# Kernel tuning notes

Hardware: AMD Instinct MI355X
Metric: run time of the kernel (lower is better)

The kernel has to match this reference:

```python
import jax, jax.numpy as jnp
import numpy as np

C_REG = 50.0  # soft-SVM regularization from __init__ default C=50


def kronecker(A, B):
    # torch: einsum('ab,cd->acbd').view(a*c, b*d)
    return jnp.einsum('ab,cd->acbd', A, B).reshape(
        A.shape[0] * B.shape[0], A.shape[1] * B.shape[1])


def setup_inputs() -> dict:
    key = jax.random.key(0)
    k1, k2, k3, k4 = jax.random.split(key, 4)
    N_c, N_S, N_Q, C, W, H = 16, 25, 15, 3, 32, 32
    D_feat = 640
    S_k = jax.random.normal(k1, (N_c, N_S, C, W, H), dtype=jnp.float32)
    Q_k = jax.random.normal(k2, (N_c, N_Q, C, W, H), dtype=jnp.float32)
    # base_net modeled as Flatten -> Linear(C*W*H, D_feat), no bias
    W_base = jax.random.normal(k3, (C * W * H, D_feat), dtype=jnp.float32) * 0.02
    gamma = jax.random.normal(k4, (1,), dtype=jnp.float32)
    return {"S_k": S_k, "Q_k": Q_k, "W_base": W_base, "gamma": gamma}


def reference(S_k, Q_k, W_base, gamma):
    N_c, N_S = S_k.shape[:2]
    N_Q = Q_k.shape[1]
    # base_net: flatten image dims, project to features
    f_x = S_k.reshape(N_c * N_S, -1) @ W_base  # placeholder
    f_x = Q_k.reshape(N_c * N_Q, -1) @ W_base          # [N_c*N_Q, D]
    K = S_k.reshape(N_c * N_S, -1) @ W_base            # [N_c*N_S, D]
    # kernel matrix + ridge
    aul = K @ K.T + C_REG * jnp.eye(N_c * N_S, dtype=K.dtype)  # [N_c*N_S, N_c*N_S]
    # explicit Kronecker expansion to the full (N_c^2*N_S) system
    Q = kronecker(jnp.eye(N_c, dtype=K.dtype), aul)    # [N_c^2*N_S, N_c^2*N_S]
    p = kronecker(jnp.eye(N_c, dtype=K.dtype),
                  jnp.ones((1, N_S), dtype=K.dtype)).reshape(-1, 1)
    alpha = jnp.linalg.solve(Q, jax.lax.stop_gradient(p))  # p is detached in torch
    alpha = alpha.reshape(N_c, -1)                     # [N_c, N_c*N_S]
    w_k = alpha @ K                                    # [N_c, D]
    logits = -gamma * (f_x @ w_k.T)                    # [N_c*N_Q, N_c]
    return logits
```

## Files before the change

kernel.cpp:

```cpp
#include <hip/hip_runtime.h>
#include <math.h>

#define DIN 3072
#define DF 640
#define MROWS 400
#define QROWS 240
#define NMAT 400
#define PN 416
#define NRHS 16
#define CREG 50.0f
#define PVSTEPS 5
#define CSTEPS 25
#define KSPLIT 8
#define GBLK 13
#define SCOLS 32
#define FPAD 72
#define MTILES 28
#define DPAD 424

typedef __attribute__((ext_vector_type(8))) short bf8v;
typedef __attribute__((ext_vector_type(4))) short s4v;
typedef __attribute__((ext_vector_type(4))) float f32x4;

__device__ __forceinline__ short bf16_rn(float x) {
  unsigned u = __float_as_uint(x);
  u += 0x7FFFu + ((u >> 16) & 1u);
  return (short)(u >> 16);
}
__device__ __forceinline__ void split_sh(float x, short& h, short& l) {
  h = bf16_rn(x);
  float hf = __uint_as_float(((unsigned)(unsigned short)h) << 16);
  l = bf16_rn(x - hf);
}

__global__ __launch_bounds__(256) void gemm_feat_sk(const float* __restrict__ S,
                                                    const float* __restrict__ Qm,
                                                    const float* __restrict__ Wb,
                                                    float* __restrict__ Acc) {
  __shared__ short Ash[128][FPAD];
  __shared__ short Asl[128][FPAD];
  __shared__ short Bsh[128][FPAD];
  __shared__ short Bsl[128][FPAD];
  int tid = threadIdx.x;
  int wave = tid >> 6, lane = tid & 63, l16 = lane & 15, quad = lane >> 4;
  int wr = wave >> 1, wc = wave & 1;
  int by = blockIdx.y, bx = blockIdx.x, bz = blockIdx.z;
  int colBase = bx * 128;
  int kbeg = bz * (DIN / KSPLIT), kend = kbeg + (DIN / KSPLIT);
  int kc4 = (tid & 15) * 4;
  float4 ar4[8], br4[8];
  auto load_regs = [&](int kk) {
#pragma unroll
    for (int p = 0; p < 8; ++p) {
      int ar_ = by * 128 + (tid >> 4) + 16 * p;
      const float* srp = (ar_ < MROWS) ? (S + (size_t)ar_ * DIN)
                                       : (Qm + (size_t)(ar_ - MROWS) * DIN);
      ar4[p] = *reinterpret_cast<const float4*>(srp + kk + kc4);
      int kr = (tid >> 4) + 16 * (p & 3);
      int cb = colBase + (p >> 2) * 64 + kc4;
      br4[p] = *reinterpret_cast<const float4*>(Wb + (size_t)(kk + kr) * DF + cb);
    }
  };
  auto split_write = [&]() {
#pragma unroll
    for (int p = 0; p < 8; ++p) {
      int row = (tid >> 4) + 16 * p;
      s4v hv, lv; short h, l;
      split_sh(ar4[p].x, h, l); hv[0] = h; lv[0] = l;
      split_sh(ar4[p].y, h, l); hv[1] = h; lv[1] = l;
      split_sh(ar4[p].z, h, l); hv[2] = h; lv[2] = l;
      split_sh(ar4[p].w, h, l); hv[3] = h; lv[3] = l;
      *reinterpret_cast<s4v*>(&Ash[row][kc4]) = hv;
      *reinterpret_cast<s4v*>(&Asl[row][kc4]) = lv;
      int kr = (tid >> 4) + 16 * (p & 3);
      int cb = (p >> 2) * 64 + kc4;
      split_sh(br4[p].x, h, l); Bsh[cb + 0][kr] = h; Bsl[cb + 0][kr] = l;
      split_sh(br4[p].y, h, l); Bsh[cb + 1][kr] = h; Bsl[cb + 1][kr] = l;
      split_sh(br4[p].z, h, l); Bsh[cb + 2][kr] = h; Bsl[cb + 2][kr] = l;
      split_sh(br4[p].w, h, l); Bsh[cb + 3][kr] = h; Bsl[cb + 3][kr] = l;
    }
  };
  f32x4 acc[4][4];
#pragma unroll
  for (int m = 0; m < 4; ++m)
#pragma unroll
    for (int n = 0; n < 4; ++n) acc[m][n] = {0, 0, 0, 0};
  load_regs(kbeg);
  split_write();
  __syncthreads();
  int k0 = kbeg;
  while (true) {
    int kn = k0 + 64;
    bool more = (kn < kend);
    if (more) load_regs(kn);
#pragma unroll
    for (int kk = 0; kk < 64; kk += 32) {
      int ko = kk + quad * 8;
      bf8v ah[4], al[4], bh[4], bl[4];
#pragma unroll
      for (int m = 0; m < 4; ++m) {
        ah[m] = *reinterpret_cast<const bf8v*>(&Ash[wr * 64 + m * 16 + l16][ko]);
        al[m] = *reinterpret_cast<const bf8v*>(&Asl[wr * 64 + m * 16 + l16][ko]);
      }
#pragma unroll
      for (int n = 0; n < 4; ++n) {
        bh[n] = *reinterpret_cast<const bf8v*>(&Bsh[wc * 64 + n * 16 + l16][ko]);
        bl[n] = *reinterpret_cast<const bf8v*>(&Bsl[wc * 64 + n * 16 + l16][ko]);
      }
#pragma unroll
      for (int m = 0; m < 4; ++m)
#pragma unroll
        for (int n = 0; n < 4; ++n) {
          acc[m][n] = __builtin_amdgcn_mfma_f32_16x16x32_bf16(ah[m], bh[n], acc[m][n], 0, 0, 0);
          acc[m][n] = __builtin_amdgcn_mfma_f32_16x16x32_bf16(ah[m], bl[n], acc[m][n], 0, 0, 0);
          acc[m][n] = __builtin_amdgcn_mfma_f32_16x16x32_bf16(al[m], bh[n], acc[m][n], 0, 0, 0);
        }
    }
    if (!more) break;
    __syncthreads();
    split_write();
    __syncthreads();
    k0 = kn;
  }
  float* Ap = Acc + (size_t)bz * 640 * DF;
#pragma unroll
  for (int m = 0; m < 4; ++m)
#pragma unroll
    for (int n = 0; n < 4; ++n)
#pragma unroll
      for (int r = 0; r < 4; ++r) {
        int row = by * 128 + wr * 64 + m * 16 + quad * 4 + r;
        int col = colBase + wc * 64 + n * 16 + l16;
        Ap[(size_t)row * DF + col] = acc[m][n][r];
      }
}

__global__ __launch_bounds__(256) void feat_reduce(const float* __restrict__ Acc,
                                                   short* __restrict__ Kh,
                                                   short* __restrict__ Kl,
                                                   float* __restrict__ FX,
                                                   float* __restrict__ zbuf,
                                                   float* __restrict__ out) {
  int tid = threadIdx.x;
  if (blockIdx.x == 0) {
    if (tid < 16) zbuf[tid] = 0.f;
  } else if (blockIdx.x == 1) {
    for (int e = tid; e < QROWS * NRHS; e += 256) out[e] = 0.f;
  }
  int idx = blockIdx.x * 256 + tid;
  if (idx >= 640 * DF) return;
  float v = 0.f;
#pragma unroll
  for (int s = 0; s < KSPLIT; ++s) v += Acc[idx + (size_t)s * 409600];
  int row = idx / DF, col = idx - row * DF;
  if (row < MROWS) {
    short h, l; split_sh(v, h, l);
    Kh[(size_t)row * DF + col] = h;
    Kl[(size_t)row * DF + col] = l;
  } else {
    FX[(size_t)(row - MROWS) * DF + col] = v;
  }
}

__global__ __launch_bounds__(256) void gemm_aul(const short* __restrict__ Kh,
                                                const short* __restrict__ Kl,
                                                short* __restrict__ Aph,
                                                short* __restrict__ Apl) {
  int tid = threadIdx.x;
  int wave = tid >> 6, lane = tid & 63;
  int l16 = lane & 15, quad = lane >> 4;
  int row0 = blockIdx.y * 64 + wave * 16;
  int colBase = blockIdx.x * 64;
  bool aValid = (row0 < MROWS);
  const bf8v bzero = {0,0,0,0,0,0,0,0};
  f32x4 acc[4] = {{0,0,0,0},{0,0,0,0},{0,0,0,0},{0,0,0,0}};
  for (int k0 = 0; k0 < DF; k0 += 32) {
    int ka = k0 + quad * 8;
    bf8v ah = bzero, al = bzero;
    if (aValid) {
      size_t ao = (size_t)(row0 + l16) * DF + ka;
      ah = *reinterpret_cast<const bf8v*>(Kh + ao);
      al = *reinterpret_cast<const bf8v*>(Kl + ao);
    }
#pragma unroll
    for (int t = 0; t < 4; ++t) {
      int colt = colBase + t * 16;
      bf8v bh = bzero, bl = bzero;
      if (colt < MROWS) {
        size_t bo = (size_t)(colt + l16) * DF + ka;
        bh = *reinterpret_cast<const bf8v*>(Kh + bo);
        bl = *reinterpret_cast<const bf8v*>(Kl + bo);
      }
      acc[t] = __builtin_amdgcn_mfma_f32_16x16x32_bf16(ah, bh, acc[t], 0, 0, 0);
      acc[t] = __builtin_amdgcn_mfma_f32_16x16x32_bf16(ah, bl, acc[t], 0, 0, 0);
      acc[t] = __builtin_amdgcn_mfma_f32_16x16x32_bf16(al, bh, acc[t], 0, 0, 0);
    }
  }
  if (row0 >= PN) return;
#pragma unroll
  for (int t = 0; t < 4; ++t) {
    int colt = colBase + t * 16;
    if (colt >= PN) continue;
#pragma unroll
    for (int r = 0; r < 4; ++r) {
      int row = row0 + quad * 4 + r;
      int col = colt + l16;
      float v = acc[t][r];
      if (row == col && row < MROWS) v += CREG;
      short h, l; split_sh(v, h, l);
      size_t o = (size_t)row * PN + col;
      Aph[o] = h; Apl[o] = l;
    }
  }
}

__global__ __launch_bounds__(256) void solve_and_m(const short* __restrict__ Aph,
                                                   const short* __restrict__ Apl,
                                                   const float* __restrict__ FX,
                                                   const short* __restrict__ Kh,
                                                   const short* __restrict__ Kl,
                                                   const float* __restrict__ gamma,
                                                   unsigned* __restrict__ D0,
                                                   unsigned* __restrict__ D1,
                                                   float* __restrict__ V0,
                                                   float* __restrict__ V1,
                                                   unsigned* __restrict__ bar,
                                                   unsigned* __restrict__ mflag,
                                                   float* __restrict__ M,
                                                   float* __restrict__ out) {
  int tid = threadIdx.x, b = blockIdx.x;
  int wave = tid >> 6, lane = tid & 63, l16 = lane & 15, quad = lane >> 4;
  const bf8v bzero = {0,0,0,0,0,0,0,0};

  if (b >= GBLK) {
    int mt = b - GBLK;
    int mb = mt / 7, nb = mt - (mt / 7) * 7;
    int q0 = mb * 64 + wave * 16;
    f32x4 acc[4] = {{0,0,0,0},{0,0,0,0},{0,0,0,0},{0,0,0,0}};
    int arow = q0 + l16;
    bool aOk = (arow < QROWS);
    const float* fr = FX + (size_t)(aOk ? arow : 0) * DF;
    for (int k0 = 0; k0 < DF; k0 += 32) {
      int ka = k0 + quad * 8;
      bf8v ah = bzero, al = bzero;
      if (aOk) {
        float4 a0 = *reinterpret_cast<const float4*>(fr + ka);
        float4 a1 = *reinterpret_cast<const float4*>(fr + ka + 4);
        float av[8] = {a0.x, a0.y, a0.z, a0.w, a1.x, a1.y, a1.z, a1.w};
#pragma unroll
        for (int j = 0; j < 8; ++j) { short h, l; split_sh(av[j], h, l); ah[j] = h; al[j] = l; }
      }
#pragma unroll
      for (int t = 0; t < 4; ++t) {
        int n = nb * 64 + t * 16 + l16;
        bf8v bh = bzero, bl = bzero;
        if (n < NMAT) {
          bh = *reinterpret_cast<const bf8v*>(Kh + (size_t)n * DF + ka);
          bl = *reinterpret_cast<const bf8v*>(Kl + (size_t)n * DF + ka);
        }
        acc[t] = __builtin_amdgcn_mfma_f32_16x16x32_bf16(ah, bh, acc[t], 0, 0, 0);
        acc[t] = __builtin_amdgcn_mfma_f32_16x16x32_bf16(ah, bl, acc[t], 0, 0, 0);
        acc[t] = __builtin_amdgcn_mfma_f32_16x16x32_bf16(al, bh, acc[t], 0, 0, 0);
      }
    }
#pragma unroll
    for (int t = 0; t < 4; ++t)
#pragma unroll
      for (int r = 0; r < 4; ++r) {
        int row = q0 + quad * 4 + r;
        int col = nb * 64 + t * 16 + l16;
        if (row < QROWS && col < NMAT)
          __hip_atomic_store(&M[(size_t)row * NMAT + col], acc[t][r],
                             __ATOMIC_RELAXED, __HIP_MEMORY_SCOPE_AGENT);
      }
    __syncthreads();
    if (tid == 0)
      __hip_atomic_fetch_add(mflag, 1u, __ATOMIC_RELEASE, __HIP_MEMORY_SCOPE_AGENT);
    return;
  }

  __shared__ __align__(16) short Abig[2][SCOLS][DPAD];
  __shared__ __align__(16) short dbT[2][NRHS][DPAD];
  __shared__ float yred[4][SCOLS][17];
  __shared__ float vprevL[PN], vcurL[PN];
  __shared__ float XsL[SCOLS][NRHS + 1];
  __shared__ float scal[2];
  __shared__ float rn[4], rd[4];
  int r0 = b * SCOLS;

  for (int e = tid; e < SCOLS * 52; e += 256) {
    int i = e / 52, c = e - i * 52;
    *reinterpret_cast<bf8v*>(&Abig[0][i][c * 8]) =
        *reinterpret_cast<const bf8v*>(Aph + (size_t)(r0 + i) * PN + c * 8);
    *reinterpret_cast<bf8v*>(&Abig[1][i][c * 8]) =
        *reinterpret_cast<const bf8v*>(Apl + (size_t)(r0 + i) * PN + c * 8);
  }
  for (int e = tid; e < NRHS * DPAD; e += 256) {
    (&dbT[0][0][0])[e] = 0; (&dbT[1][0][0])[e] = 0;
  }
  for (int e = tid; e < PN; e += 256) {
    float v = (e < NMAT) ? (1.f + 0.125f * (float)(e & 7)) : 0.f;
    vcurL[e] = v;
    dbT[0][0][e] = bf16_rn(v);
  }
  __syncthreads();

  unsigned ph = 0;
  auto gridbar = [&]() {
    __syncthreads();
    ++ph;
    if (tid == 0) {
      unsigned tgt = ph * GBLK;
      __hip_atomic_fetch_add(bar, 1u, __ATOMIC_RELEASE, __HIP_MEMORY_SCOPE_AGENT);
      while (__hip_atomic_load(bar, __ATOMIC_RELAXED, __HIP_MEMORY_SCOPE_AGENT) < tgt)
        __builtin_amdgcn_s_sleep(2);
    }
    __syncthreads();
  };

  auto matvec = [&](bool lo) {
    f32x4 acc0 = {0, 0, 0, 0}, acc1 = {0, 0, 0, 0};
    for (int kt = wave; kt < 13; kt += 4) {
      int ko = kt * 32 + quad * 8;
      bf8v bh = *reinterpret_cast<const bf8v*>(&dbT[0][l16][ko]);
      bf8v ah0 = *reinterpret_cast<const bf8v*>(&Abig[0][l16][ko]);
      bf8v ah1 = *reinterpret_cast<const bf8v*>(&Abig[0][16 + l16][ko]);
      acc0 = __builtin_amdgcn_mfma_f32_16x16x32_bf16(ah0, bh, acc0, 0, 0, 0);
      acc1 = __builtin_amdgcn_mfma_f32_16x16x32_bf16(ah1, bh, acc1, 0, 0, 0);
      if (lo) {
        bf8v bl = *reinterpret_cast<const bf8v*>(&dbT[1][l16][ko]);
        bf8v al0 = *reinterpret_cast<const bf8v*>(&Abig[1][l16][ko]);
        bf8v al1 = *reinterpret_cast<const bf8v*>(&Abig[1][16 + l16][ko]);
        acc0 = __builtin_amdgcn_mfma_f32_16x16x32_bf16(ah0, bl, acc0, 0, 0, 0);
        acc0 = __builtin_amdgcn_mfma_f32_16x16x32_bf16(al0, bh, acc0, 0, 0, 0);
        acc1 = __builtin_amdgcn_mfma_f32_16x16x32_bf16(ah1, bl, acc1, 0, 0, 0);
        acc1 = __builtin_amdgcn_mfma_f32_16x16x32_bf16(al1, bh, acc1, 0, 0, 0);
      }
    }
#pragma unroll
    for (int r_ = 0; r_ < 4; ++r_) {
      yred[wave][quad * 4 + r_][l16] = acc0[r_];
      yred[wave][16 + quad * 4 + r_][l16] = acc1[r_];
    }
  };

  for (int s = 0; s < PVSTEPS; ++s) {
    matvec(false);
    __syncthreads();
    if (tid < SCOLS) {
      float y = yred[0][tid][0] + yred[1][tid][0] + yred[2][tid][0] + yred[3][tid][0];
      float* Vb = (s & 1) ? V1 : V0;
      __hip_atomic_store(&Vb[r0 + tid], y, __ATOMIC_RELAXED, __HIP_MEMORY_SCOPE_AGENT);
    }
    gridbar();
    const float* Vb = (s & 1) ? V1 : V0;
    if (s == PVSTEPS - 1)
      for (int e = tid; e < PN; e += 256) vprevL[e] = vcurL[e];
    float g0 = __hip_atomic_load((float*)&Vb[tid], __ATOMIC_RELAXED, __HIP_MEMORY_SCOPE_AGENT);
    float g1 = (tid < PN - 256)
        ? __hip_atomic_load((float*)&Vb[tid + 256], __ATOMIC_RELAXED, __HIP_MEMORY_SCOPE_AGENT)
        : 0.f;
    {
      float v = g0 * (1.f / 4096.f);
      vcurL[tid] = v;
      dbT[0][0][tid] = bf16_rn(v);
    }
    if (tid < PN - 256) {
      float v = g1 * (1.f / 4096.f);
      vcurL[tid + 256] = v;
      dbT[0][0][tid + 256] = bf16_rn(v);
    }
    __syncthreads();
  }

  {
    float n = 0.f, dd = 0.f;
    for (int e = tid; e < PN; e += 256) {
      n += vprevL[e] * vcurL[e];
      dd += vprevL[e] * vprevL[e];
    }
#pragma unroll
    for (int o = 32; o; o >>= 1) {
      n += __shfl_down(n, o);
      dd += __shfl_down(dd, o);
    }
    if (lane == 0) { rn[wave] = n; rd[wave] = dd; }
    __syncthreads();
    if (tid == 0) {
      float N = rn[0] + rn[1] + rn[2] + rn[3];
      float D = rd[0] + rd[1] + rd[2] + rd[3];
      float rqv = 4096.f * N / D;
      float bb = 1.3f * rqv;
      if (!(bb > 800.f)) bb = 12000.f;
      if (bb > 100000.f) bb = 100000.f;
      scal[0] = 0.5f * (bb + CREG);
      scal[1] = 0.5f * (bb - CREG);
    }
    __syncthreads();
  }
  float theta = scal[0], delta = scal[1];
  float sigma = theta / delta, rho = 1.f / sigma;

  float xr[2], rr[2], dr[2];
#pragma unroll
  for (int m = 0; m < 2; ++m) {
    int rl = (tid >> 4) + 16 * m, c = tid & 15, gi = r0 + rl;
    float pc = (gi < NMAT && (gi / 25) == c) ? 1.f : 0.f;
    xr[m] = 0.f; rr[m] = pc; dr[m] = pc / theta;
    short h, l; split_sh(dr[m], h, l);
    __hip_atomic_store(&D0[(size_t)gi * NRHS + c],
                       ((unsigned)(unsigned short)h << 16) | (unsigned)(unsigned short)l,
                       __ATOMIC_RELAXED, __HIP_MEMORY_SCOPE_AGENT);
  }
  gridbar();
  {
    unsigned gw[26];
#pragma unroll
    for (int j = 0; j < 26; ++j)
      gw[j] = __hip_atomic_load(&D0[tid + 256 * j], __ATOMIC_RELAXED, __HIP_MEMORY_SCOPE_AGENT);
#pragma unroll
    for (int j = 0; j < 26; ++j) {
      int e = tid + 256 * j, row = e >> 4, c = e & 15;
      dbT[0][c][row] = (short)(gw[j] >> 16);
      dbT[1][c][row] = (short)gw[j];
    }
  }
  __syncthreads();

  for (int k = 0; k < CSTEPS - 1; ++k) {
    matvec(true);
    __syncthreads();
    float rho1 = 1.f / (2.f * sigma - rho);
    float s1 = rho1 * rho, s2 = 2.f * rho1 / delta;
    rho = rho1;
    unsigned* Db = (k & 1) ? D0 : D1;
#pragma unroll
    for (int m = 0; m < 2; ++m) {
      int rl = (tid >> 4) + 16 * m, c = tid & 15, gi = r0 + rl;
      float mv = yred[0][rl][c] + yred[1][rl][c] + yred[2][rl][c] + yred[3][rl][c];
      xr[m] += dr[m];
      rr[m] -= mv;
      float dn = s1 * dr[m] + s2 * rr[m];
      dr[m] = dn;
      if (k < CSTEPS - 2) {
        short h, l; split_sh(dn, h, l);
        __hip_atomic_store(&Db[(size_t)gi * NRHS + c],
                           ((unsigned)(unsigned short)h << 16) | (unsigned)(unsigned short)l,
                           __ATOMIC_RELAXED, __HIP_MEMORY_SCOPE_AGENT);
      }
    }
    if (k < CSTEPS - 2) {
      gridbar();
      unsigned gw[26];
#pragma unroll
      for (int j = 0; j < 26; ++j)
        gw[j] = __hip_atomic_load(&Db[tid + 256 * j], __ATOMIC_RELAXED, __HIP_MEMORY_SCOPE_AGENT);
#pragma unroll
      for (int j = 0; j < 26; ++j) {
        int e = tid + 256 * j, row = e >> 4, c = e & 15;
        dbT[0][c][row] = (short)(gw[j] >> 16);
        dbT[1][c][row] = (short)gw[j];
      }
    }
    __syncthreads();
  }

#pragma unroll
  for (int m = 0; m < 2; ++m) {
    int rl = (tid >> 4) + 16 * m, c = tid & 15;
    XsL[rl][c] = xr[m] + dr[m];
  }
  __syncthreads();
  if (tid == 0) {
    while (__hip_atomic_load(mflag, __ATOMIC_RELAXED, __HIP_MEMORY_SCOPE_AGENT) < MTILES)
      __builtin_amdgcn_s_sleep(2);
  }
  __syncthreads();
  float* Msl = reinterpret_cast<float*>(&Abig[0][0][0]);
  {
    float gm[30];
#pragma unroll
    for (int j = 0; j < 30; ++j) {
      int e = tid + 256 * j;
      int q = e >> 5, i = e & 31;
      gm[j] = (r0 + i < NMAT)
                  ? __hip_atomic_load(&M[(size_t)q * NMAT + r0 + i],
                                      __ATOMIC_RELAXED, __HIP_MEMORY_SCOPE_AGENT)
                  : 0.f;
    }
#pragma unroll
    for (int j = 0; j < 30; ++j) Msl[tid + 256 * j] = gm[j];
  }
  __syncthreads();
  float g = -gamma[0];
  int c = tid & 15;
  for (int q = tid >> 4; q < QROWS; q += 16) {
    float s = 0.f;
#pragma unroll
    for (int i = 0; i < SCOLS; ++i) s += Msl[q * SCOLS + i] * XsL[i][c];
    atomicAdd(&out[q * NRHS + c], g * s);
  }
}

extern "C" void kernel_launch(void* const* d_in, const int* in_sizes, int n_in,
                              void* d_out, int out_size, void* d_ws, size_t ws_size,
                              hipStream_t stream) {
  const float* S = (const float*)d_in[0];
  const float* Qm = (const float*)d_in[1];
  const float* Wb = (const float*)d_in[2];
  const float* gamma = (const float*)d_in[3];
  float* out = (float*)d_out;
  char* base = (char*)d_ws;
  short* Kh   = (short*)(base);
  short* Kl   = (short*)(base + 512000);
  float* FX   = (float*)(base + 1024000);
  short* Aph  = (short*)(base + 1638400);
  short* Apl  = (short*)(base + 1984512);
  float* Mm   = (float*)(base + 2330624);
  unsigned* bar = (unsigned*)(base + 2740224);
  unsigned* mflag = (unsigned*)(base + 2740240);
  float* zbuf = (float*)(base + 2740224);
  unsigned* D0 = (unsigned*)(base + 2740288);
  unsigned* D1 = (unsigned*)(base + 2766912);
  float* V0   = (float*)(base + 2793536);
  float* V1   = (float*)(base + 2795200);
  float* Acc  = (float*)(base + 2796864);

  gemm_feat_sk<<<dim3(5, 5, KSPLIT), 256, 0, stream>>>(S, Qm, Wb, Acc);
  feat_reduce<<<1600, 256, 0, stream>>>(Acc, Kh, Kl, FX, zbuf, out);
  gemm_aul<<<dim3(7, 7), 256, 0, stream>>>(Kh, Kl, Aph, Apl);
  solve_and_m<<<GBLK + MTILES, 256, 0, stream>>>(Aph, Apl, FX, Kh, Kl, gamma,
                                                 D0, D1, V0, V1, bar, mflag,
                                                 Mm, out);
}
```

Before: 209.4 us.

## Pre-split inputs and weights to bf16 hi/lo in a separate kernel with swizzled LDS

Adds a presplit kernel that converts S/Q rows and a transposed W_base into bf16 hi/lo arrays in global memory, so the feature GEMM loads bf16 directly instead of splitting fp32 inside every block. The GEMM's LDS layout switches from padded arrays to XOR-swizzled 64-wide rows, loaded with 16-byte vectors. The zero-init work moves from feat_reduce into the new kernel. The cost is an extra launch plus extra global traffic to write and reread about 16MB of split data. The gain is that each tile is no longer split redundantly across blocks and the strided transposed LDS stores go away.

Measured after the change: 211.0 us. About the same (+0.8%).

```diff
diff --git a/kernel.cpp b/kernel.cpp
--- a/kernel.cpp
+++ b/kernel.cpp
@@ -14,7 +14,6 @@
 #define KSPLIT 8
 #define GBLK 13
 #define SCOLS 32
-#define FPAD 72
 #define MTILES 28
 #define DPAD 424
 
@@ -33,51 +32,92 @@
   l = bf16_rn(x - hf);
 }
 
-__global__ __launch_bounds__(256) void gemm_feat_sk(const float* __restrict__ S,
-                                                    const float* __restrict__ Qm,
-                                                    const float* __restrict__ Wb,
+__global__ __launch_bounds__(256) void presplit(const float* __restrict__ S,
+                                                const float* __restrict__ Qm,
+                                                const float* __restrict__ Wb,
+                                                short* __restrict__ ATh,
+                                                short* __restrict__ ATl,
+                                                short* __restrict__ WTh,
+                                                short* __restrict__ WTl,
+                                                float* __restrict__ zbuf,
+                                                float* __restrict__ out) {
+  int b = blockIdx.x, tid = threadIdx.x;
+  if (b < 960) {
+    int ci = b * 256 + tid;
+    int row = ci / 384, rem = ci - row * 384;
+    const float* sr = (row < MROWS) ? (S + (size_t)row * DIN)
+                                    : (Qm + (size_t)(row - MROWS) * DIN);
+    float4 a0 = *reinterpret_cast<const float4*>(sr + rem * 8);
+    float4 a1 = *reinterpret_cast<const float4*>(sr + rem * 8 + 4);
+    float av[8] = {a0.x, a0.y, a0.z, a0.w, a1.x, a1.y, a1.z, a1.w};
+    bf8v hv, lv;
+#pragma unroll
+    for (int j = 0; j < 8; ++j) { short h, l; split_sh(av[j], h, l); hv[j] = h; lv[j] = l; }
+    size_t o = (size_t)row * DIN + rem * 8;
+    *reinterpret_cast<bf8v*>(ATh + o) = hv;
+    *reinterpret_cast<bf8v*>(ATl + o) = lv;
+    return;
+  }
+  if (b >= 1440) {
+    if (b == 1440) { if (tid < 16) zbuf[tid] = 0.f; }
+    else { for (int e = tid; e < QROWS * NRHS; e += 256) out[e] = 0.f; }
+    return;
+  }
+  __shared__ short tH[64][68];
+  __shared__ short tL[64][68];
+  int b2 = b - 960;
+  int kt = b2 % 48, ct = b2 / 48;
+  int k0 = kt * 64, c0 = ct * 64;
+#pragma unroll
+  for (int p = 0; p < 16; ++p) {
+    int idx = p * 256 + tid;
+    int i = idx >> 6, j = idx & 63;
+    float v = Wb[(size_t)(k0 + i) * DF + c0 + j];
+    short h, l; split_sh(v, h, l);
+    tH[i][j] = h; tL[i][j] = l;
+  }
+  __syncthreads();
+#pragma unroll
+  for (int p = 0; p < 16; ++p) {
+    int idx = p * 256 + tid;
+    int j = idx >> 6, i = idx & 63;
+    WTh[(size_t)(c0 + j) * DIN + k0 + i] = tH[i][j];
+    WTl[(size_t)(c0 + j) * DIN + k0 + i] = tL[i][j];
+  }
+}
+
+__global__ __launch_bounds__(256) void gemm_feat_sk(const short* __restrict__ ATh,
+                                                    const short* __restrict__ ATl,
+                                                    const short* __restrict__ WTh,
+                                                    const short* __restrict__ WTl,
                                                     float* __restrict__ Acc) {
-  __shared__ short Ash[128][FPAD];
-  __shared__ short Asl[128][FPAD];
-  __shared__ short Bsh[128][FPAD];
-  __shared__ short Bsl[128][FPAD];
+  __shared__ __align__(16) short Ahs[8192];
+  __shared__ __align__(16) short Als[8192];
+  __shared__ __align__(16) short Bhs[8192];
+  __shared__ __align__(16) short Bls[8192];
   int tid = threadIdx.x;
   int wave = tid >> 6, lane = tid & 63, l16 = lane & 15, quad = lane >> 4;
   int wr = wave >> 1, wc = wave & 1;
   int by = blockIdx.y, bx = blockIdx.x, bz = blockIdx.z;
-  int colBase = bx * 128;
   int kbeg = bz * (DIN / KSPLIT), kend = kbeg + (DIN / KSPLIT);
-  int kc4 = (tid & 15) * 4;
-  float4 ar4[8], br4[8];
+  int lrow = tid >> 3, lc = tid & 7;
+  bf8v rg[16];
   auto load_regs = [&](int kk) {
 #pragma unroll
-    for (int p = 0; p < 8; ++p) {
-      int ar_ = by * 128 + (tid >> 4) + 16 * p;
-      const float* srp = (ar_ < MROWS) ? (S + (size_t)ar_ * DIN)
-                                       : (Qm + (size_t)(ar_ - MROWS) * DIN);
-      ar4[p] = *reinterpret_cast<const float4*>(srp + kk + kc4);
-      int kr = (tid >> 4) + 16 * (p & 3);
-      int cb = colBase + (p >> 2) * 64 + kc4;
-      br4[p] = *reinterpret_cast<const float4*>(Wb + (size_t)(kk + kr) * DF + cb);
+    for (int it = 0; it < 16; ++it) {
+      int row = (it & 3) * 32 + lrow;
+      const short* base = (it < 4) ? ATh : (it < 8) ? ATl : (it < 12) ? WTh : WTl;
+      int grow = ((it < 8) ? by : bx) * 128 + row;
+      rg[it] = *reinterpret_cast<const bf8v*>(base + (size_t)grow * DIN + kk + lc * 8);
     }
   };
-  auto split_write = [&]() {
-#pragma unroll
-    for (int p = 0; p < 8; ++p) {
-      int row = (tid >> 4) + 16 * p;
-      s4v hv, lv; short h, l;
-      split_sh(ar4[p].x, h, l); hv[0] = h; lv[0] = l;
-      split_sh(ar4[p].y, h, l); hv[1] = h; lv[1] = l;
-      split_sh(ar4[p].z, h, l); hv[2] = h; lv[2] = l;
-      split_sh(ar4[p].w, h, l); hv[3] = h; lv[3] = l;
-      *reinterpret_cast<s4v*>(&Ash[row][kc4]) = hv;
-      *reinterpret_cast<s4v*>(&Asl[row][kc4]) = lv;
-      int kr = (tid >> 4) + 16 * (p & 3);
-      int cb = (p >> 2) * 64 + kc4;
-      split_sh(br4[p].x, h, l); Bsh[cb + 0][kr] = h; Bsl[cb + 0][kr] = l;
-      split_sh(br4[p].y, h, l); Bsh[cb + 1][kr] = h; Bsl[cb + 1][kr] = l;
-      split_sh(br4[p].z, h, l); Bsh[cb + 2][kr] = h; Bsl[cb + 2][kr] = l;
-      split_sh(br4[p].w, h, l); Bsh[cb + 3][kr] = h; Bsl[cb + 3][kr] = l;
+  auto store_lds = [&]() {
+    int sc = (lc ^ (lrow & 7)) << 3;
+#pragma unroll
+    for (int it = 0; it < 16; ++it) {
+      int row = (it & 3) * 32 + lrow;
+      short* lb = (it < 4) ? Ahs : (it < 8) ? Als : (it < 12) ? Bhs : Bls;
+      *reinterpret_cast<bf8v*>(&lb[row * 64 + sc]) = rg[it];
     }
   };
   f32x4 acc[4][4];
@@ -86,7 +126,7 @@
 #pragma unroll
     for (int n = 0; n < 4; ++n) acc[m][n] = {0, 0, 0, 0};
   load_regs(kbeg);
-  split_write();
+  store_lds();
   __syncthreads();
   int k0 = kbeg;
   while (true) {
@@ -95,17 +135,21 @@
     if (more) load_regs(kn);
 #pragma unroll
     for (int kk = 0; kk < 64; kk += 32) {
-      int ko = kk + quad * 8;
+      int chunk = (kk >> 3) + quad;
       bf8v ah[4], al[4], bh[4], bl[4];
 #pragma unroll
       for (int m = 0; m < 4; ++m) {
-        ah[m] = *reinterpret_cast<const bf8v*>(&Ash[wr * 64 + m * 16 + l16][ko]);
-        al[m] = *reinterpret_cast<const bf8v*>(&Asl[wr * 64 + m * 16 + l16][ko]);
+        int row = wr * 64 + m * 16 + l16;
+        int sc = (chunk ^ (row & 7)) << 3;
+        ah[m] = *reinterpret_cast<const bf8v*>(&Ahs[row * 64 + sc]);
+        al[m] = *reinterpret_cast<const bf8v*>(&Als[row * 64 + sc]);
       }
 #pragma unroll
       for (int n = 0; n < 4; ++n) {
-        bh[n] = *reinterpret_cast<const bf8v*>(&Bsh[wc * 64 + n * 16 + l16][ko]);
-        bl[n] = *reinterpret_cast<const bf8v*>(&Bsl[wc * 64 + n * 16 + l16][ko]);
+        int col = wc * 64 + n * 16 + l16;
+        int sc = (chunk ^ (col & 7)) << 3;
+        bh[n] = *reinterpret_cast<const bf8v*>(&Bhs[col * 64 + sc]);
+        bl[n] = *reinterpret_cast<const bf8v*>(&Bls[col * 64 + sc]);
       }
 #pragma unroll
       for (int m = 0; m < 4; ++m)
@@ -118,7 +162,7 @@
     }
     if (!more) break;
     __syncthreads();
-    split_write();
+    store_lds();
     __syncthreads();
     k0 = kn;
   }
@@ -130,7 +174,7 @@
 #pragma unroll
       for (int r = 0; r < 4; ++r) {
         int row = by * 128 + wr * 64 + m * 16 + quad * 4 + r;
-        int col = colBase + wc * 64 + n * 16 + l16;
+        int col = bx * 128 + wc * 64 + n * 16 + l16;
         Ap[(size_t)row * DF + col] = acc[m][n][r];
       }
 }
@@ -138,16 +182,8 @@
 __global__ __launch_bounds__(256) void feat_reduce(const float* __restrict__ Acc,
                                                    short* __restrict__ Kh,
                                                    short* __restrict__ Kl,
-                                                   float* __restrict__ FX,
-                                                   float* __restrict__ zbuf,
-                                                   float* __restrict__ out) {
-  int tid = threadIdx.x;
-  if (blockIdx.x == 0) {
-    if (tid < 16) zbuf[tid] = 0.f;
-  } else if (blockIdx.x == 1) {
-    for (int e = tid; e < QROWS * NRHS; e += 256) out[e] = 0.f;
-  }
-  int idx = blockIdx.x * 256 + tid;
+                                                   float* __restrict__ FX) {
+  int idx = blockIdx.x * 256 + threadIdx.x;
   if (idx >= 640 * DF) return;
   float v = 0.f;
 #pragma unroll
@@ -524,10 +560,15 @@
   unsigned* D1 = (unsigned*)(base + 2766912);
   float* V0   = (float*)(base + 2793536);
   float* V1   = (float*)(base + 2795200);
-  float* Acc  = (float*)(base + 2796864);
-
-  gemm_feat_sk<<<dim3(5, 5, KSPLIT), 256, 0, stream>>>(S, Qm, Wb, Acc);
-  feat_reduce<<<1600, 256, 0, stream>>>(Acc, Kh, Kl, FX, zbuf, out);
+  short* ATh  = (short*)(base + 2796864);
+  short* ATl  = (short*)(base + 6729024);
+  short* WTh  = (short*)(base + 10661184);
+  short* WTl  = (short*)(base + 14593344);
+  float* Acc  = (float*)(base + 18525504);
+
+  presplit<<<1442, 256, 0, stream>>>(S, Qm, Wb, ATh, ATl, WTh, WTl, zbuf, out);
+  gemm_feat_sk<<<dim3(5, 5, KSPLIT), 256, 0, stream>>>(ATh, ATl, WTh, WTl, Acc);
+  feat_reduce<<<1600, 256, 0, stream>>>(Acc, Kh, Kl, FX);
   gemm_aul<<<dim3(7, 7), 256, 0, stream>>>(Kh, Kl, Aph, Apl);
   solve_and_m<<<GBLK + MTILES, 256, 0, stream>>>(Aph, Apl, FX, Kh, Kl, gamma,
                                                  D0, D1, V0, V1, bar, mflag,
```
